# Kernel tuning notes

Measured on AMD Instinct MI355X. Metric: run time of the kernel, lower is better.

## Reference

```python
import jax, jax.numpy as jnp
import numpy as np

COMP_TOKEN_ID = 7
R = 8
LORA_ALPHA = 16
SCALING = LORA_ALPHA / R  # 2.0


def setup_inputs() -> dict:
    key = jax.random.key(0)
    k1, k2, k3, k4, k5, k6 = jax.random.split(key, 6)
    B, S, D_IN, D_OUT = 4, 4096, 4096, 4096
    x = jax.random.normal(k1, (B, S, D_IN), dtype=jnp.float32)
    ids = jax.random.randint(k2, (B, S), 0, 64, dtype=jnp.int64)
    W = jax.random.normal(k3, (D_OUT, D_IN), dtype=jnp.float32) * (1.0 / np.sqrt(D_IN))
    b = jax.random.normal(k4, (D_OUT,), dtype=jnp.float32) * 0.02
    lora_A = jax.random.normal(k5, (R, D_IN), dtype=jnp.float32) * (1.0 / np.sqrt(D_IN))
    lora_B = jax.random.normal(k6, (D_OUT, R), dtype=jnp.float32) * 0.02
    return {"x": x, "ids": ids, "W": W, "b": b, "lora_A": lora_A, "lora_B": lora_B}


def reference(x, ids, W, b, lora_A, lora_B):
    # Base frozen linear: [B,S,d_in] @ [d_in,d_out] -> [B,S,d_out]
    base = jnp.einsum('bsi,oi->bso', x, W) + b
    # LoRA path (dropout is identity in eval mode): x @ A.T @ B.T * scaling
    lora = jnp.einsum('bsr,or->bso', jnp.einsum('bsi,ri->bsr', x, lora_A), lora_B) * SCALING
    # Per-token gate: only compression tokens get the LoRA update
    mask = (ids == COMP_TOKEN_ID).astype(x.dtype)[..., None]  # [B,S,1]
    return base + lora * mask
```

## Files before the change

### kernel.cpp

```cpp
#include <hip/hip_runtime.h>
#include <hip/hip_bf16.h>
#include <stdint.h>


typedef __attribute__((ext_vector_type(8))) __bf16 bf16x8;
typedef __attribute__((ext_vector_type(4))) float f32x4;

#define M_DIM 16384
#define K_DIM 4096
#define N_DIM 4096
#define BM 256
#define BN 256
#define BK 64
#define NT2 (K_DIM / BK)

__global__ void cvt_f32_bf16(const float* __restrict__ in, __hip_bfloat16* __restrict__ out, int n8) {
    int i = blockIdx.x * blockDim.x + threadIdx.x;
    int stride = gridDim.x * blockDim.x;
    for (; i < n8; i += stride) {
        const float4* p = (const float4*)(in + (size_t)i * 8);
        float4 v0 = p[0], v1 = p[1];
        bf16x8 o;
        o[0] = (__bf16)v0.x; o[1] = (__bf16)v0.y; o[2] = (__bf16)v0.z; o[3] = (__bf16)v0.w;
        o[4] = (__bf16)v1.x; o[5] = (__bf16)v1.y; o[6] = (__bf16)v1.z; o[7] = (__bf16)v1.w;
        *(bf16x8*)((__hip_bfloat16*)out + (size_t)i * 8) = o;
    }
}

__global__ void compute_xa(const __hip_bfloat16* __restrict__ Xb,
                           const int* __restrict__ ids,
                           const float* __restrict__ A,
                           float* __restrict__ xa) {
    int t = threadIdx.x;
    int r = t & 63;
    int kq = t >> 6;
    int row = blockIdx.x * 64 + r;
    const __hip_bfloat16* xrow = Xb + (size_t)row * K_DIM + kq * 1024;
    float acc[8] = {0.f, 0.f, 0.f, 0.f, 0.f, 0.f, 0.f, 0.f};
    for (int i = 0; i < 128; i++) {
        bf16x8 xv = *(const bf16x8*)(xrow + i * 8);
        int kk = kq * 1024 + i * 8;
#pragma unroll
        for (int rr = 0; rr < 8; rr++) {
            const float* ap = A + rr * K_DIM + kk;
            float4 a0 = *(const float4*)ap;
            float4 a1 = *(const float4*)(ap + 4);
            acc[rr] += (float)xv[0] * a0.x + (float)xv[1] * a0.y + (float)xv[2] * a0.z + (float)xv[3] * a0.w
                     + (float)xv[4] * a1.x + (float)xv[5] * a1.y + (float)xv[6] * a1.z + (float)xv[7] * a1.w;
        }
    }
    __shared__ float red[4][64][8];
#pragma unroll
    for (int rr = 0; rr < 8; rr++) red[kq][r][rr] = acc[rr];
    __syncthreads();
    if (t < 64) {
        int rowg = blockIdx.x * 64 + t;
        float gate = (ids[rowg] == 7) ? 2.0f : 0.0f;
#pragma unroll
        for (int rr = 0; rr < 8; rr++) {
            float s = (red[0][t][rr] + red[1][t][rr]) + (red[2][t][rr] + red[3][t][rr]);
            xa[(size_t)rowg * 8 + rr] = s * gate;
        }
    }
}

__device__ __forceinline__ void gload_lds16(const void* g, void* l) {
    __builtin_amdgcn_global_load_lds(
        (const __attribute__((address_space(1))) unsigned int*)g,
        (__attribute__((address_space(3))) unsigned int*)l, 16, 0, 0);
}

#define LGKMW(n) asm volatile("s_waitcnt lgkmcnt(" #n ")" ::: "memory")
#define VMCW(n)  asm volatile("s_waitcnt vmcnt(" #n ")" ::: "memory")
#define SB0()    __builtin_amdgcn_sched_barrier(0)
#define BAR()    __builtin_amdgcn_s_barrier()
#define PRIO(p)  __builtin_amdgcn_s_setprio(p)

__global__ __launch_bounds__(512, 1) void gemm_bias_lora(
    const __hip_bfloat16* __restrict__ Xb,
    const __hip_bfloat16* __restrict__ Wb,
    const float* __restrict__ bias,
    const float* __restrict__ xa,
    const float* __restrict__ loraB,
    float* __restrict__ out) {
    __shared__ char smem[2 * 65536];

    int tid = threadIdx.x;
    int bid = blockIdx.x;
    int swz = (bid & 7) * 128 + (bid >> 3);
    int n_tile = swz & 15;
    int m_tile = swz >> 4;
    int m_base = m_tile * BM, n_base = n_tile * BN;
    int wave = tid >> 6, lane = tid & 63;
    int wr = wave >> 2, wc = wave & 3;
    int l15 = lane & 15, lhi = lane >> 4;
    int l8 = lane >> 3;
    int cx = ((lane & 7) ^ l8) * 16;
    int pswz0 = ((lhi)     ^ (l15 & 7)) * 16;
    int pswz1 = ((4 + lhi) ^ (l15 & 7)) * 16;

    f32x4 acc[8][4] = {};

    const char* Abase = (const char*)(Xb + (size_t)m_base * K_DIM);
    const char* Bbase = (const char*)(Wb + (size_t)n_base * K_DIM);

    auto stage_A = [&](int kt, int mq, int buf) {
        char* ub = smem + buf * 65536 + mq * 16384;
#pragma unroll
        for (int j = 0; j < 2; j++) {
            int rg = wave * 2 + j;
            int rl = rg * 8 + l8;
            int g = (rl < 64) ? (mq * 64 + rl) : (128 + mq * 64 + (rl - 64));
            gload_lds16(Abase + (size_t)g * (K_DIM * 2) + (size_t)kt * 128 + cx,
                        ub + rg * 1024 + lane * 16);
        }
    };
    auto stage_B = [&](int kt, int h, int buf) {
        char* ub = smem + buf * 65536 + 32768 + h * 16384;
#pragma unroll
        for (int j = 0; j < 2; j++) {
            int rg = wave * 2 + j;
            int row = h * 128 + rg * 8 + l8;
            gload_lds16(Bbase + (size_t)row * (K_DIM * 2) + (size_t)kt * 128 + cx,
                        ub + rg * 1024 + lane * 16);
        }
    };

    stage_A(0, 0, 0); stage_B(0, 0, 0); stage_B(0, 1, 0); stage_A(0, 1, 0);
    stage_A(1, 0, 1);
    VMCW(2);
    BAR();

    bf16x8 af0[4], af1[4], bf0[4], bf1[4];

    for (int t = 0; t < NT2; t++) {
        int cur = t & 1, nb = cur ^ 1;
        const char* aU0 = smem + cur * 65536 + (wr * 64 + l15) * 128;
        const char* aU1 = aU0 + 16384;
        const char* bRb = smem + cur * 65536 + 32768 + (wc * 64 + l15) * 128;

#pragma unroll
        for (int mi = 0; mi < 4; mi++) af0[mi] = *(const bf16x8*)(aU0 + mi * 2048 + pswz0);
#pragma unroll
        for (int ni = 0; ni < 4; ni++) bf0[ni] = *(const bf16x8*)(bRb + ni * 2048 + pswz0);
#pragma unroll
        for (int mi = 0; mi < 4; mi++) af1[mi] = *(const bf16x8*)(aU1 + mi * 2048 + pswz0);
        if (t + 1 < NT2) stage_B(t + 1, 0, nb);
        LGKMW(4); SB0();
        PRIO(1);
#pragma unroll
        for (int mi = 0; mi < 4; mi++)
#pragma unroll
            for (int ni = 0; ni < 4; ni++)
                acc[mi][ni] = __builtin_amdgcn_mfma_f32_16x16x32_bf16(af0[mi], bf0[ni], acc[mi][ni], 0, 0, 0);
        PRIO(0);

#pragma unroll
        for (int mi = 0; mi < 4; mi++) af0[mi] = *(const bf16x8*)(aU0 + mi * 2048 + pswz1);
#pragma unroll
        for (int ni = 0; ni < 4; ni++) bf1[ni] = *(const bf16x8*)(bRb + ni * 2048 + pswz1);
        if (t + 1 < NT2) { stage_B(t + 1, 1, nb); stage_A(t + 1, 1, nb); }
        LGKMW(8); SB0();
        PRIO(1);
#pragma unroll
        for (int mi = 0; mi < 4; mi++)
#pragma unroll
            for (int ni = 0; ni < 4; ni++)
                acc[4 + mi][ni] = __builtin_amdgcn_mfma_f32_16x16x32_bf16(af1[mi], bf0[ni], acc[4 + mi][ni], 0, 0, 0);
        PRIO(0);

#pragma unroll
        for (int mi = 0; mi < 4; mi++) af1[mi] = *(const bf16x8*)(aU1 + mi * 2048 + pswz1);
        LGKMW(4); SB0();
        PRIO(1);
#pragma unroll
        for (int mi = 0; mi < 4; mi++)
#pragma unroll
            for (int ni = 0; ni < 4; ni++)
                acc[mi][ni] = __builtin_amdgcn_mfma_f32_16x16x32_bf16(af0[mi], bf1[ni], acc[mi][ni], 0, 0, 0);
        PRIO(0);
        BAR();

        if (t + 2 < NT2) stage_A(t + 2, 0, cur);
        LGKMW(0); SB0();
        PRIO(1);
#pragma unroll
        for (int mi = 0; mi < 4; mi++)
#pragma unroll
            for (int ni = 0; ni < 4; ni++)
                acc[4 + mi][ni] = __builtin_amdgcn_mfma_f32_16x16x32_bf16(af1[mi], bf1[ni], acc[4 + mi][ni], 0, 0, 0);
        PRIO(0);
        if (t < NT2 - 2) { VMCW(2); } else { VMCW(0); }
        BAR();
    }

    int wrow = m_base + wr * 128;
    int wcol = n_base + wc * 64;
    float bv[4];
    float4 lb0[4], lb1[4];
#pragma unroll
    for (int ni = 0; ni < 4; ni++) {
        int n = wcol + ni * 16 + l15;
        bv[ni] = bias[n];
        lb0[ni] = *(const float4*)(loraB + (size_t)n * 8);
        lb1[ni] = *(const float4*)(loraB + (size_t)n * 8 + 4);
    }
#pragma unroll
    for (int mi = 0; mi < 8; mi++) {
#pragma unroll
        for (int r = 0; r < 4; r++) {
            int m = wrow + mi * 16 + lhi * 4 + r;
            float4 xa0 = *(const float4*)(xa + (size_t)m * 8);
            float4 xa1 = *(const float4*)(xa + (size_t)m * 8 + 4);
#pragma unroll
            for (int ni = 0; ni < 4; ni++) {
                int n = wcol + ni * 16 + l15;
                float lora = xa0.x * lb0[ni].x + xa0.y * lb0[ni].y + xa0.z * lb0[ni].z + xa0.w * lb0[ni].w
                           + xa1.x * lb1[ni].x + xa1.y * lb1[ni].y + xa1.z * lb1[ni].z + xa1.w * lb1[ni].w;
                out[(size_t)m * N_DIM + n] = acc[mi][ni][r] + bv[ni] + lora;
            }
        }
    }
}

__global__ void fallback_kernel(const float* __restrict__ x, const int* __restrict__ ids,
                                const float* __restrict__ W, const float* __restrict__ b,
                                const float* __restrict__ A, const float* __restrict__ B8,
                                float* __restrict__ out) {
    __shared__ float xs[K_DIM];
    __shared__ float xa_s[8];
    int row = blockIdx.y;
    int t = threadIdx.x;
    const float* xr = x + (size_t)row * K_DIM;
    for (int k = t; k < K_DIM; k += 256) xs[k] = xr[k];
    __syncthreads();
    if (t < 8) {
        float s = 0.f;
        for (int k = 0; k < K_DIM; k++) s += xs[k] * A[t * K_DIM + k];
        xa_s[t] = (ids[row] == 7) ? s * 2.0f : 0.0f;
    }
    __syncthreads();
    int col = blockIdx.x * 256 + t;
    const float* wr = W + (size_t)col * K_DIM;
    float acc = 0.f;
    for (int k = 0; k < K_DIM; k++) acc += xs[k] * wr[k];
    float lora = 0.f;
#pragma unroll
    for (int rr = 0; rr < 8; rr++) lora += xa_s[rr] * B8[col * 8 + rr];
    out[(size_t)row * N_DIM + col] = acc + b[col] + lora;
}

extern "C" void kernel_launch(void* const* d_in, const int* in_sizes, int n_in,
                              void* d_out, int out_size, void* d_ws, size_t ws_size,
                              hipStream_t stream) {
    const float* x   = (const float*)d_in[0];
    const int*   ids = (const int*)d_in[1];
    const float* W   = (const float*)d_in[2];
    const float* b   = (const float*)d_in[3];
    const float* lA  = (const float*)d_in[4];
    const float* lB  = (const float*)d_in[5];
    float* out = (float*)d_out;

    size_t wb_bytes = (size_t)N_DIM * K_DIM * 2;
    size_t xb_bytes = (size_t)M_DIM * K_DIM * 2;
    size_t xa_bytes = (size_t)M_DIM * 8 * 4;

    if (ws_size >= wb_bytes + xb_bytes + xa_bytes) {
        __hip_bfloat16* Wb = (__hip_bfloat16*)d_ws;
        __hip_bfloat16* Xb = (__hip_bfloat16*)((char*)d_ws + wb_bytes);
        float* xa = (float*)((char*)d_ws + wb_bytes + xb_bytes);

        cvt_f32_bf16<<<1024, 256, 0, stream>>>(W, Wb, (int)((size_t)N_DIM * K_DIM / 8));
        cvt_f32_bf16<<<2048, 256, 0, stream>>>(x, Xb, (int)((size_t)M_DIM * K_DIM / 8));
        compute_xa<<<M_DIM / 64, 256, 0, stream>>>(Xb, ids, lA, xa);
        gemm_bias_lora<<<(M_DIM / BM) * (N_DIM / BN), 512, 0, stream>>>(Xb, Wb, b, xa, lB, out);
    } else {
        fallback_kernel<<<dim3(N_DIM / 256, M_DIM), 256, 0, stream>>>(x, ids, W, b, lA, lB, out);
    }
}
```

Measured before the change: 654.2 us.

## Triple-buffer first A quarter-tile in LDS to drop mid-iteration barrier

Reworks the LDS layout so the first A sub-tile uses a three-slot ring buffer while the second A half and the B tile stay double-buffered. Because the prefetch of tile t+2's A quarter now goes into a slot nobody is still reading, the workgroup barrier before that prefetch is removed, leaving one barrier per K iteration. The cost is 16 KB more LDS (144 KB total) and some modular slot bookkeeping.

Measured after the change: 654.0 us. Within noise of the previous version (-0.0%).

```diff
diff --git a/kernel.cpp b/kernel.cpp
--- a/kernel.cpp
+++ b/kernel.cpp
@@ -83,7 +83,7 @@
     const float* __restrict__ xa,
     const float* __restrict__ loraB,
     float* __restrict__ out) {
-    __shared__ char smem[2 * 65536];
+    __shared__ char smem[147456];
 
     int tid = threadIdx.x;
     int bid = blockIdx.x;
@@ -104,19 +104,18 @@
     const char* Abase = (const char*)(Xb + (size_t)m_base * K_DIM);
     const char* Bbase = (const char*)(Wb + (size_t)n_base * K_DIM);
 
-    auto stage_A = [&](int kt, int mq, int buf) {
-        char* ub = smem + buf * 65536 + mq * 16384;
+    auto stage_Au = [&](int kt, int mq, char* ubase) {
 #pragma unroll
         for (int j = 0; j < 2; j++) {
             int rg = wave * 2 + j;
             int rl = rg * 8 + l8;
             int g = (rl < 64) ? (mq * 64 + rl) : (128 + mq * 64 + (rl - 64));
             gload_lds16(Abase + (size_t)g * (K_DIM * 2) + (size_t)kt * 128 + cx,
-                        ub + rg * 1024 + lane * 16);
+                        ubase + rg * 1024 + lane * 16);
         }
     };
     auto stage_B = [&](int kt, int h, int buf) {
-        char* ub = smem + buf * 65536 + 32768 + h * 16384;
+        char* ub = smem + 81920 + buf * 32768 + h * 16384;
 #pragma unroll
         for (int j = 0; j < 2; j++) {
             int rg = wave * 2 + j;
@@ -126,18 +125,22 @@
         }
     };
 
-    stage_A(0, 0, 0); stage_B(0, 0, 0); stage_B(0, 1, 0); stage_A(0, 1, 0);
-    stage_A(1, 0, 1);
+    stage_Au(0, 0, smem);
+    stage_B(0, 0, 0); stage_B(0, 1, 0);
+    stage_Au(0, 1, smem + 49152);
+    stage_Au(1, 0, smem + 16384);
     VMCW(2);
     BAR();
 
     bf16x8 af0[4], af1[4], bf0[4], bf1[4];
+    int s0 = 0;
 
     for (int t = 0; t < NT2; t++) {
-        int cur = t & 1, nb = cur ^ 1;
-        const char* aU0 = smem + cur * 65536 + (wr * 64 + l15) * 128;
-        const char* aU1 = aU0 + 16384;
-        const char* bRb = smem + cur * 65536 + 32768 + (wc * 64 + l15) * 128;
+        int cb = t & 1, nb = cb ^ 1;
+        int s2 = s0 + 2; if (s2 >= 3) s2 -= 3;
+        const char* aU0 = smem + s0 * 16384 + (wr * 64 + l15) * 128;
+        const char* aU1 = smem + 49152 + cb * 16384 + (wr * 64 + l15) * 128;
+        const char* bRb = smem + 81920 + cb * 32768 + (wc * 64 + l15) * 128;
 
 #pragma unroll
         for (int mi = 0; mi < 4; mi++) af0[mi] = *(const bf16x8*)(aU0 + mi * 2048 + pswz0);
@@ -159,7 +162,7 @@
         for (int mi = 0; mi < 4; mi++) af0[mi] = *(const bf16x8*)(aU0 + mi * 2048 + pswz1);
 #pragma unroll
         for (int ni = 0; ni < 4; ni++) bf1[ni] = *(const bf16x8*)(bRb + ni * 2048 + pswz1);
-        if (t + 1 < NT2) { stage_B(t + 1, 1, nb); stage_A(t + 1, 1, nb); }
+        if (t + 1 < NT2) { stage_B(t + 1, 1, nb); stage_Au(t + 1, 1, smem + 49152 + nb * 16384); }
         LGKMW(8); SB0();
         PRIO(1);
 #pragma unroll
@@ -179,9 +182,8 @@
             for (int ni = 0; ni < 4; ni++)
                 acc[mi][ni] = __builtin_amdgcn_mfma_f32_16x16x32_bf16(af0[mi], bf1[ni], acc[mi][ni], 0, 0, 0);
         PRIO(0);
-        BAR();
-
-        if (t + 2 < NT2) stage_A(t + 2, 0, cur);
+
+        if (t + 2 < NT2) stage_Au(t + 2, 0, smem + s2 * 16384);
         LGKMW(0); SB0();
         PRIO(1);
 #pragma unroll
@@ -192,6 +194,8 @@
         PRIO(0);
         if (t < NT2 - 2) { VMCW(2); } else { VMCW(0); }
         BAR();
+
+        s0 = s0 + 1; if (s0 >= 3) s0 -= 3;
     }
 
     int wrow = m_base + wr * 128;
```
